# Kernel optimization log

Hardware: AMD Instinct MI355X
Metric: run time of the kernel (lower is better)

The kernel has to match this reference:

```python
import jax, jax.numpy as jnp
import numpy as np

N = 10000        # nodes
E = 160000       # graph edges (avg degree 16)
EI = 100000      # interaction edges
EP = 50000       # positive interaction edges
EA = 50000       # a2b edges
H, D = 4, 128    # GAT heads, per-head (and per-layer) dim
F_IN, F_EDGE = 39, 27   # 17+19+3 node feats, 27 edge feats
EMB = 256
FCN_IN = F_IN + 3 * D + D  # 551: x stacked with 3 GAT outputs + GCN output

PARAM_SHAPES = []
for l, fin in enumerate([F_IN, D, D]):
    PARAM_SHAPES += [(f"gat{l}_W", (fin, H * D)), (f"gat{l}_We", (F_EDGE, H * D)),
                     (f"gat{l}_asrc", (H, D)), (f"gat{l}_adst", (H, D)),
                     (f"gat{l}_aedge", (H, D)), (f"gat{l}_b", (D,))]
PARAM_SHAPES += [("gcn_W", (D, D)), ("gcn_b", (D,))]
for nm, fi, hh, fo in [("fcn", FCN_IN, 1024, EMB), ("link", 2 * EMB + 2, 1024, 1),
                       ("a2b", 2 * EMB, 1024, 6), ("node", EMB, 1024, 16),
                       ("int", 2 * EMB + 2, 1024, 3)]:
    PARAM_SHAPES += [(f"{nm}_W1", (fi, hh)), (f"{nm}_b1", (hh,)),
                     (f"{nm}_g", (hh,)), (f"{nm}_be", (hh,)),
                     (f"{nm}_W2", (hh, fo)), (f"{nm}_b2", (fo,))]
PARAM_NAMES = [n for n, _ in PARAM_SHAPES]


def setup_inputs():
    ks = jax.random.split(jax.random.key(0), len(PARAM_SHAPES) + 10)
    inp = {
        "x": jax.random.normal(ks[0], (N, F_IN), jnp.float32),
        "edge_index": jax.random.randint(ks[1], (2, E), 0, N),
        "edge_attr": jax.random.normal(ks[2], (E, F_EDGE), jnp.float32),
        "interaction_edge_index_pos": jax.random.randint(ks[3], (2, EP), 0, N),
        "interaction_edge_index": jax.random.randint(ks[4], (2, EI), 0, N),
        "xyz_data": jax.random.normal(ks[5], (N, 3), jnp.float32),
        "vector_data": jax.random.normal(ks[6], (N, 3), jnp.float32),
        "a2b_index": jax.random.randint(ks[7], (2, EA), 0, N),
        "mask": jnp.zeros((1,), jnp.float32),  # only used by the (disabled) evolver path
    }
    for i, (name, shp) in enumerate(PARAM_SHAPES):
        if name.endswith("_g"):
            inp[name] = jnp.ones(shp, jnp.float32)        # BatchNorm gamma
        elif name.endswith(("_be", "_b", "_b1", "_b2")):
            inp[name] = jnp.zeros(shp, jnp.float32)       # biases / BN beta
        else:
            inp[name] = jax.random.normal(ks[10 + i], shp, jnp.float32) * 0.05
    return inp


def _bn(h, g, b, eps=1e-5):
    # BatchNorm1d in training mode: biased batch statistics over axis 0
    m = h.mean(0)
    v = ((h - m) ** 2).mean(0)
    return (h - m) * jax.lax.rsqrt(v + eps) * g + b


def _seg_softmax(logits, seg, n):
    m = jax.ops.segment_max(logits, seg, num_segments=n)
    e = jnp.exp(logits - m[seg])
    s = jax.ops.segment_sum(e, seg, num_segments=n)
    return e / (s[seg] + 1e-16)


def _cos(a, b, eps=1e-8):
    na = jnp.maximum(jnp.sqrt((a * a).sum(1)), eps)
    nb = jnp.maximum(jnp.sqrt((b * b).sum(1)), eps)
    return (a * b).sum(1) / (na * nb)


def _forward(x, edge_attr, xyz_data, vector_data, edge_index, iep, iei, a2b_index, params):
    p = dict(zip(PARAM_NAMES, params))
    n = x.shape[0]
    src, dst = edge_index[0], edge_index[1]
    loops = jnp.arange(n)
    # GATConv add_self_loops with fill_value='mean': per-node mean of incoming edge_attr
    cnt = jax.ops.segment_sum(jnp.ones(src.shape[0], x.dtype), dst, num_segments=n)
    loop_attr = jax.ops.segment_sum(edge_attr, dst, num_segments=n) / jnp.maximum(cnt, 1.0)[:, None]
    src_a = jnp.concatenate([src, loops])
    dst_a = jnp.concatenate([dst, loops])
    ea_a = jnp.concatenate([edge_attr, loop_attr], 0)

    def gat(xx, W, We, asrc, adst, aedge, b):
        h = (xx @ W).reshape(n, H, D)
        a_s = (h * asrc).sum(-1)                               # [n,H]
        a_d = (h * adst).sum(-1)                               # [n,H]
        a_e = ((ea_a @ We).reshape(-1, H, D) * aedge).sum(-1)  # [E',H]
        alpha = jax.nn.leaky_relu(a_s[src_a] + a_d[dst_a] + a_e, 0.2)
        alpha = _seg_softmax(alpha, dst_a, n)                  # softmax over incoming edges
        out = jax.ops.segment_sum(h[src_a] * alpha[:, :, None], dst_a, num_segments=n)
        return out.mean(1) + b                                 # concat=False -> mean over heads

    out = x
    steps = [x]
    for l in range(3):
        out = jax.nn.relu(gat(out, p[f"gat{l}_W"], p[f"gat{l}_We"], p[f"gat{l}_asrc"],
                              p[f"gat{l}_adst"], p[f"gat{l}_aedge"], p[f"gat{l}_b"]))
        steps.append(out)
    # GCNConv: self loops (weight 1) + symmetric normalization
    deg = jax.ops.segment_sum(jnp.ones(dst_a.shape[0], x.dtype), dst_a, num_segments=n)
    dinv = jnp.where(deg > 0, deg ** -0.5, 0.0)
    norm = dinv[src_a] * dinv[dst_a]
    hg = out @ p["gcn_W"]
    out = jax.ops.segment_sum(hg[src_a] * norm[:, None], dst_a, num_segments=n) + p["gcn_b"]
    steps.append(out)

    feat = jnp.concatenate(steps, 1)                           # [n, 551]
    h = jax.nn.relu(feat @ p["fcn_W1"] + p["fcn_b1"])
    h = _bn(h, p["fcn_g"], p["fcn_be"])
    emb = jax.nn.relu(h @ p["fcn_W2"] + p["fcn_b2"])           # [n, 256]

    def head(z, nm):
        hh = jax.nn.relu(z @ p[f"{nm}_W1"] + p[f"{nm}_b1"])
        hh = _bn(hh, p[f"{nm}_g"], p[f"{nm}_be"])
        return hh @ p[f"{nm}_W2"] + p[f"{nm}_b2"]

    def pair_feat(idx):
        z = jnp.concatenate([emb[idx[0]], emb[idx[1]]], 1)
        d = ((xyz_data[idx[0]] - xyz_data[idx[1]]) ** 2).sum(1)  # squared distance (no sqrt)
        a = _cos(vector_data[idx[0]], vector_data[idx[1]])
        return jnp.concatenate([z, d[:, None], a[:, None]], 1)

    link_preds = head(pair_feat(iei), "link")
    a2b_preds = head(jnp.concatenate([emb[a2b_index[0]], emb[a2b_index[1]]], 1), "a2b")
    node_preds = head(emb, "node")
    int_preds = head(pair_feat(iep), "int")
    return (link_preds, a2b_preds, node_preds, int_preds)


def reference(x, edge_index, edge_attr, interaction_edge_index_pos, interaction_edge_index,
              xyz_data, vector_data, a2b_index, mask,
              gat0_W, gat0_We, gat0_asrc, gat0_adst, gat0_aedge, gat0_b,
              gat1_W, gat1_We, gat1_asrc, gat1_adst, gat1_aedge, gat1_b,
              gat2_W, gat2_We, gat2_asrc, gat2_adst, gat2_aedge, gat2_b,
              gcn_W, gcn_b,
              fcn_W1, fcn_b1, fcn_g, fcn_be, fcn_W2, fcn_b2,
              link_W1, link_b1, link_g, link_be, link_W2, link_b2,
              a2b_W1, a2b_b1, a2b_g, a2b_be, a2b_W2, a2b_b2,
              node_W1, node_b1, node_g, node_be, node_W2, node_b2,
              int_W1, int_b1, int_g, int_be, int_W2, int_b2):
    loc = locals()
    params = tuple(loc[nm] for nm in PARAM_NAMES)
    return _forward(x, edge_attr, xyz_data, vector_data, edge_index,
                    interaction_edge_index_pos, interaction_edge_index, a2b_index, params)
```

## Files before the change

kernel.cpp:

```cpp
#include <hip/hip_runtime.h>
#include <hip/hip_bf16.h>
#include <cstdint>
#include <cstddef>

typedef __attribute__((ext_vector_type(8))) short bf16x8;
typedef __attribute__((ext_vector_type(4))) float f32x4;

__device__ inline float bf2f(unsigned short u) {
    union { float f; unsigned int i; } c; c.i = ((unsigned int)u) << 16; return c.f;
}
__device__ inline unsigned short f2b(float v) {
    __hip_bfloat16 h = __float2bfloat16(v);
    union { __hip_bfloat16 b; unsigned short u; } c; c.b = h; return c.u;
}

__device__ inline float wmax64(float v) {
    #pragma unroll
    for (int o = 32; o; o >>= 1) v = fmaxf(v, __shfl_xor(v, o));
    return v;
}
__device__ inline float wsum64(float v) {
    #pragma unroll
    for (int o = 32; o; o >>= 1) v += __shfl_xor(v, o);
    return v;
// ... 33 lines not shown
            int idx = t * CH + j;
            if (idx < nn) coff[idx] = base + loc[j];
        }
    }
    if (t == 1023) coff[nn] = part[1023];
}

__global__ void k_fill(const int* __restrict__ dst, const int* __restrict__ coff,
                       int* __restrict__ fill, int* __restrict__ ceid, int E_) {
    int e = blockIdx.x * 256 + threadIdx.x;
    if (e < E_) {
        int d = dst[e];
        int p = atomicAdd(&fill[d], 1);
        ceid[coff[d] + p] = e;
    }
}

__global__ void k_copy_x(const float* __restrict__ x, float* __restrict__ feat, int nn) {
    int t = blockIdx.x * 256 + threadIdx.x;
    if (t < nn * 39) feat[(size_t)(t / 39) * 551 + (t % 39)] = x[t];
}

__global__ __launch_bounds__(128) void k_loopattr(const float* __restrict__ ea, const int* __restrict__ coff,
                                                  const int* __restrict__ ceid, float* __restrict__ la, int nn) {
    int g = blockIdx.x * 4 + (threadIdx.x >> 5);
    int lane = threadIdx.x & 31;
    if (g >= nn || lane >= 27) return;
    int beg = coff[g], cnt = coff[g + 1] - beg;
    float v = 0.f;
    for (int e = 0; e < cnt; ++e) v += ea[(size_t)ceid[beg + e] * 27 + lane];
// ... 15 lines not shown
    if (r >= E_ + nn) return;
    const float* src = (r < E_) ? (ea + (size_t)r * 27) : (la + (size_t)(r - E_) * 27);
    float o0 = 0, o1 = 0, o2 = 0, o3 = 0;
    #pragma unroll
    for (int f = 0; f < 27; ++f) {
        float xv = src[f];
        o0 += xv * Wea[f * 4 + 0];
        o1 += xv * Wea[f * 4 + 1];
        o2 += xv * Wea[f * 4 + 2];
        o3 += xv * Wea[f * 4 + 3];
    }
    a_e[(size_t)r * 4 + 0] = o0; a_e[(size_t)r * 4 + 1] = o1;
    a_e[(size_t)r * 4 + 2] = o2; a_e[(size_t)r * 4 + 3] = o3;
}

__global__ void k_asd(const float* __restrict__ h, const float* __restrict__ asrc,
                      const float* __restrict__ adst, float* __restrict__ a_s,
                      float* __restrict__ a_d, int nn) {
    int t = blockIdx.x * 256 + threadIdx.x;
    if (t >= nn * 4) return;
    int node = t >> 2, hh = t & 3;
    const float* hp = h + (size_t)node * 512 + hh * 128;
    float vs = 0.f, vd = 0.f;
    for (int d = 0; d < 128; ++d) {
        float xv = hp[d];
        vs += xv * asrc[hh * 128 + d];
        vd += xv * adst[hh * 128 + d];
    }
    a_s[t] = vs;
    a_d[t] = vd;
}

__global__ __launch_bounds__(64) void k_attn(
    const float* __restrict__ h, const float* __restrict__ a_s, const float* __restrict__ a_d,
    const float* __restrict__ a_e, const int* __restrict__ esrc,
    const int* __restrict__ coff, const int* __restrict__ ceid,
    const float* __restrict__ bvec, float* __restrict__ feat, int colofs, int E_) {
    const int i = blockIdx.x;
    const int lane = threadIdx.x;
    const int beg = coff[i];
    const int cnt = coff[i + 1] - beg;
    const int total = cnt + 1;
    const float d0 = a_d[i * 4 + 0], d1 = a_d[i * 4 + 1], d2 = a_d[i * 4 + 2], d3 = a_d[i * 4 + 3];
    float m0 = -1e30f, m1 = -1e30f, m2 = -1e30f, m3 = -1e30f;
    for (int e = lane; e < total; e += 64) {
        int eid, s;
        if (e < cnt) { eid = ceid[beg + e]; s = esrc[eid]; } else { eid = E_ + i; s = i; }
        float l0 = a_s[s * 4 + 0] + d0 + a_e[(size_t)eid * 4 + 0];
        float l1 = a_s[s * 4 + 1] + d1 + a_e[(size_t)eid * 4 + 1];
// ... 22 lines not shown
        s2 += __expf(l2 - m2); s3 += __expf(l3 - m3);
    }
    s0 = wsum64(s0); s1 = wsum64(s1); s2 = wsum64(s2); s3 = wsum64(s3);
    const int myh = lane >> 4;
    const float mm = myh == 0 ? m0 : myh == 1 ? m1 : myh == 2 ? m2 : m3;
    const float sv = myh == 0 ? s0 : myh == 1 ? s1 : myh == 2 ? s2 : s3;
    const float dd = myh == 0 ? d0 : myh == 1 ? d1 : myh == 2 ? d2 : d3;
    const float iv = 1.f / (sv + 1e-16f);
    float acc[8] = {0, 0, 0, 0, 0, 0, 0, 0};
    for (int e = 0; e < total; ++e) {
        int eid, s;
        if (e < cnt) { eid = ceid[beg + e]; s = esrc[eid]; } else { eid = E_ + i; s = i; }
        float l = a_s[s * 4 + myh] + dd + a_e[(size_t)eid * 4 + myh];
        l = l > 0.f ? l : 0.2f * l;
        const float wgt = __expf(l - mm) * iv;
        const float4* hp = (const float4*)(h + (size_t)s * 512 + lane * 8);
        float4 x0 = hp[0], x1 = hp[1];
        acc[0] += wgt * x0.x; acc[1] += wgt * x0.y; acc[2] += wgt * x0.z; acc[3] += wgt * x0.w;
        acc[4] += wgt * x1.x; acc[5] += wgt * x1.y; acc[6] += wgt * x1.z; acc[7] += wgt * x1.w;
    }
    __shared__ float sh[512];
    #pragma unroll
    for (int j = 0; j < 8; ++j) sh[lane * 8 + j] = acc[j];
    __syncthreads();
    #pragma unroll
    for (int r = 0; r < 2; ++r) {
        int d = lane * 2 + r;
        float v = 0.25f * (sh[d] + sh[128 + d] + sh[256 + d] + sh[384 + d]) + bvec[d];
        feat[(size_t)i * 551 + colofs + d] = fmaxf(v, 0.f);
    }
}

__global__ __launch_bounds__(64) void k_gcn(const float* __restrict__ hg, const int* __restrict__ esrc,
    const int* __restrict__ coff, const int* __restrict__ ceid, const int* __restrict__ indeg,
    const float* __restrict__ bvec, float* __restrict__ feat) {
    const int i = blockIdx.x;
    const int lane = threadIdx.x;
    const int beg = coff[i];
    const int cnt = coff[i + 1] - beg;
    const float di = rsqrtf((float)(indeg[i] + 1));
    const int d = lane * 2;
    float acc0 = hg[(size_t)i * 128 + d] * di;
    float acc1 = hg[(size_t)i * 128 + d + 1] * di;
    for (int e = 0; e < cnt; ++e) {
        int eid = ceid[beg + e];
        int s = esrc[eid];
        float ds = rsqrtf((float)(indeg[s] + 1));
        acc0 += hg[(size_t)s * 128 + d] * ds;
        acc1 += hg[(size_t)s * 128 + d + 1] * ds;
    }
    feat[(size_t)i * 551 + 423 + d] = acc0 * di + bvec[d];
    feat[(size_t)i * 551 + 423 + d + 1] = acc1 * di + bvec[d + 1];
}

__global__ void k_pack_ex(const int* __restrict__ idx, const float* __restrict__ xyz,
                          const float* __restrict__ vec, int4* __restrict__ pp, int P) {
    int p = blockIdx.x * 256 + threadIdx.x;
    if (p >= P) return;
    int i = idx[p], j = idx[P + p];
    float dx = xyz[i * 3] - xyz[j * 3];
    float dy = xyz[i * 3 + 1] - xyz[j * 3 + 1];
    float dz = xyz[i * 3 + 2] - xyz[j * 3 + 2];
    float d = dx * dx + dy * dy + dz * dz;
    float a0 = vec[i * 3], a1 = vec[i * 3 + 1], a2 = vec[i * 3 + 2];
    float b0 = vec[j * 3], b1 = vec[j * 3 + 1], b2 = vec[j * 3 + 2];
    float na = fmaxf(sqrtf(a0 * a0 + a1 * a1 + a2 * a2), 1e-8f);
    float nb = fmaxf(sqrtf(b0 * b0 + b1 * b1 + b2 * b2), 1e-8f);
    float a = (a0 * b0 + a1 * b1 + a2 * b2) / (na * nb);
    pp[p] = make_int4(i, j, __float_as_int(d), __float_as_int(a));
}

__global__ void k_pack2(const int* __restrict__ idx, int2* __restrict__ pp, int P) {
    int p = blockIdx.x * 256 + threadIdx.x;
    if (p >= P) return;
    pp[p] = make_int2(idx[p], idx[P + p]);
}

__global__ void k_stage_a(const float* __restrict__ src, int lds, int off,
                          unsigned short* __restrict__ dst, int ldd, int M, int K, int Mp) {
    int idx = blockIdx.x * 256 + threadIdx.x;
    if (idx >= Mp * ldd) return;
    int m = idx / ldd, k = idx - m * ldd;
    float v = (m < M && k < K) ? src[(size_t)m * lds + off + k] : 0.f;
    dst[idx] = f2b(v);
}

__global__ void k_conv_bt(const float* __restrict__ src, int ldn,
                          unsigned short* __restrict__ dst, int Kp, int K, int N, int Np) {
    int idx = blockIdx.x * 256 + threadIdx.x;
    if (idx >= Np * Kp) return;
    int nrow = idx / Kp, k = idx - nrow * Kp;
    float v = (nrow < N && k < K) ? src[(size_t)k * ldn + nrow] : 0.f;
    dst[idx] = f2b(v);
}

template<int OUT, bool RELU, bool BIAS>
__global__ __launch_bounds__(256) void gemm_mfma(
    const unsigned short* __restrict__ A, int lda,
    const unsigned short* __restrict__ Bt, int ldb,
    const float* __restrict__ bias,
    void* __restrict__ Cv, int ldc,
    int M, int N, int K) {
    const int t = threadIdx.x;
    const int lane = t & 63;
    const int wid = t >> 6;
    const int wm = wid >> 1, wn = wid & 1;
    const int bm0 = blockIdx.y * 128 + wm * 64;
// ... 93 lines not shown
        float wv = W2[(size_t)k * NO + c];
        W2f[(size_t)k * NO + c] = wv * s;
        accb += (be[k] - mv[k] * s) * wv;
    }
    red[t] = accb;
    __syncthreads();
    for (int o = 128; o; o >>= 1) {
        if (t < o) red[t] += red[t + o];
        __syncthreads();
    }
    if (t == 0) b2f[c] = b2[c] + red[0];
}

template<bool HASEX>
__global__ __launch_bounds__(256) void k_pairA(
    const unsigned short* __restrict__ u0, const unsigned short* __restrict__ u1,
    const float* __restrict__ b1, const float* __restrict__ W1ex,
    const int4* __restrict__ pp4, const int2* __restrict__ pp2,
    int P, float* __restrict__ part) {
    const int b = blockIdx.x, t = threadIdx.x;
    const int chunk = (P + 1023) / 1024;
    const int r0 = b * chunk;
    const int r1 = min(P, r0 + chunk);
    const float4 bb = *(const float4*)(b1 + t * 4);
    float4 wd = make_float4(0, 0, 0, 0), wa = make_float4(0, 0, 0, 0);
    if constexpr (HASEX) {
        wd = *(const float4*)(W1ex + t * 4);
        wa = *(const float4*)(W1ex + 1024 + t * 4);
    }
    float s[4] = {0, 0, 0, 0}, ss[4] = {0, 0, 0, 0};
    int r = r0;
    for (; r + 1 < r1; r += 2) {
        int i0A, i1A, i0B, i1B;
        float dA = 0, aA = 0, dB = 0, aB = 0;
        if constexpr (HASEX) {
            const int4 rA = pp4[r], rB = pp4[r + 1];
            i0A = rA.x; i1A = rA.y; dA = __int_as_float(rA.z); aA = __int_as_float(rA.w);
            i0B = rB.x; i1B = rB.y; dB = __int_as_float(rB.z); aB = __int_as_float(rB.w);
        } else {
            const int2 rA = pp2[r], rB = pp2[r + 1];
            i0A = rA.x; i1A = rA.y; i0B = rB.x; i1B = rB.y;
        }
        const ushort4 q0A = *(const ushort4*)(u0 + (size_t)i0A * 1024 + t * 4);
        const ushort4 q1A = *(const ushort4*)(u1 + (size_t)i1A * 1024 + t * 4);
        const ushort4 q0B = *(const ushort4*)(u0 + (size_t)i0B * 1024 + t * 4);
        const ushort4 q1B = *(const ushort4*)(u1 + (size_t)i1B * 1024 + t * 4);
        float hA[4], hB[4];
        hA[0] = bf2f(q0A.x) + bf2f(q1A.x) + bb.x;
        hA[1] = bf2f(q0A.y) + bf2f(q1A.y) + bb.y;
        hA[2] = bf2f(q0A.z) + bf2f(q1A.z) + bb.z;
        hA[3] = bf2f(q0A.w) + bf2f(q1A.w) + bb.w;
        hB[0] = bf2f(q0B.x) + bf2f(q1B.x) + bb.x;
        hB[1] = bf2f(q0B.y) + bf2f(q1B.y) + bb.y;
        hB[2] = bf2f(q0B.z) + bf2f(q1B.z) + bb.z;
        hB[3] = bf2f(q0B.w) + bf2f(q1B.w) + bb.w;
        if constexpr (HASEX) {
            hA[0] += dA * wd.x + aA * wa.x; hA[1] += dA * wd.y + aA * wa.y;
            hA[2] += dA * wd.z + aA * wa.z; hA[3] += dA * wd.w + aA * wa.w;
            hB[0] += dB * wd.x + aB * wa.x; hB[1] += dB * wd.y + aB * wa.y;
            hB[2] += dB * wd.z + aB * wa.z; hB[3] += dB * wd.w + aB * wa.w;
        }
        #pragma unroll
        for (int j = 0; j < 4; ++j) {
            float hvA = fmaxf(hA[j], 0.f);
            float hvB = fmaxf(hB[j], 0.f);
            s[j] += hvA + hvB; ss[j] += hvA * hvA + hvB * hvB;
        }
    }
    if (r < r1) {
        int i0, i1;
        float d = 0, a = 0;
        if constexpr (HASEX) {
            const int4 rA = pp4[r];
            i0 = rA.x; i1 = rA.y; d = __int_as_float(rA.z); a = __int_as_float(rA.w);
        } else {
            const int2 rA = pp2[r];
            i0 = rA.x; i1 = rA.y;
        }
        const ushort4 q0 = *(const ushort4*)(u0 + (size_t)i0 * 1024 + t * 4);
        const ushort4 q1 = *(const ushort4*)(u1 + (size_t)i1 * 1024 + t * 4);
        float h[4];
        h[0] = bf2f(q0.x) + bf2f(q1.x) + bb.x;
        h[1] = bf2f(q0.y) + bf2f(q1.y) + bb.y;
        h[2] = bf2f(q0.z) + bf2f(q1.z) + bb.z;
        h[3] = bf2f(q0.w) + bf2f(q1.w) + bb.w;
        if constexpr (HASEX) {
            h[0] += d * wd.x + a * wa.x; h[1] += d * wd.y + a * wa.y;
            h[2] += d * wd.z + a * wa.z; h[3] += d * wd.w + a * wa.w;
        }
        #pragma unroll
        for (int j = 0; j < 4; ++j) {
            float hv = fmaxf(h[j], 0.f);
            s[j] += hv; ss[j] += hv * hv;
        }
    }
    #pragma unroll
    for (int j = 0; j < 4; ++j) {
        part[(size_t)b * 2048 + t * 4 + j] = s[j];
        part[(size_t)b * 2048 + 1024 + t * 4 + j] = ss[j];
    }
}

template<int NO, bool HASEX>
__global__ __launch_bounds__(256) void k_pairB(
    const unsigned short* __restrict__ u0, const unsigned short* __restrict__ u1,
    const float* __restrict__ b1, const float* __restrict__ W1ex,
    const float* __restrict__ W2f, const float* __restrict__ b2f,
    const int4* __restrict__ pp4, const int2* __restrict__ pp2,
    float* __restrict__ out, int P) {
    const int t = threadIdx.x;
    const int wid = t >> 6, lane = t & 63;
    const int p0 = (blockIdx.x * 4 + wid) * 2;
    if (p0 >= P) return;
    const int p1 = p0 + 1;
    const bool has1 = p1 < P;
    int i0A, i1A, i0B, i1B;
    float dA = 0, aA = 0, dB = 0, aB = 0;
    if constexpr (HASEX) {
        const int4 rA = pp4[p0];
        const int4 rB = pp4[has1 ? p1 : p0];
        i0A = rA.x; i1A = rA.y; dA = __int_as_float(rA.z); aA = __int_as_float(rA.w);
        i0B = rB.x; i1B = rB.y; dB = __int_as_float(rB.z); aB = __int_as_float(rB.w);
    } else {
        const int2 rA = pp2[p0];
        const int2 rB = pp2[has1 ? p1 : p0];
        i0A = rA.x; i1A = rA.y; i0B = rB.x; i1B = rB.y;
    }
    const int k0 = lane * 16;
    union U { uint4 u; unsigned short us[8]; };
    U a0A, a1A, b0A, b1A_, a0B, a1B, b0B, b1B_;
    const unsigned short* pa = u0 + (size_t)i0A * 1024 + k0;
    const unsigned short* pb = u1 + (size_t)i1A * 1024 + k0;
    const unsigned short* pc = u0 + (size_t)i0B * 1024 + k0;
    const unsigned short* pd = u1 + (size_t)i1B * 1024 + k0;
    a0A.u = *(const uint4*)(pa);     a1A.u = *(const uint4*)(pa + 8);
    b0A.u = *(const uint4*)(pb);     b1A_.u = *(const uint4*)(pb + 8);
    a0B.u = *(const uint4*)(pc);     a1B.u = *(const uint4*)(pc + 8);
    b0B.u = *(const uint4*)(pd);     b1B_.u = *(const uint4*)(pd + 8);
    float4 bbv[4];
    #pragma unroll
    for (int q = 0; q < 4; ++q) bbv[q] = *(const float4*)(b1 + k0 + q * 4);
    float4 wdv[4], wav[4];
    if constexpr (HASEX) {
        #pragma unroll
        for (int q = 0; q < 4; ++q) {
            wdv[q] = *(const float4*)(W1ex + k0 + q * 4);
            wav[q] = *(const float4*)(W1ex + 1024 + k0 + q * 4);
        }
    }
// ... 2 lines not shown
    for (int no = 0; no < NO; ++no) { accA[no] = 0.f; accB[no] = 0.f; }
    #pragma unroll
    for (int j = 0; j < 16; ++j) {
        const int q = j >> 2, c = j & 3;
        const float bbj = (&bbv[q].x)[c];
        float exA = 0.f, exB = 0.f;
        if constexpr (HASEX) {
            const float wdj = (&wdv[q].x)[c], waj = (&wav[q].x)[c];
            exA = dA * wdj + aA * waj;
            exB = dB * wdj + aB * waj;
        }
        const float hAv = (j < 8 ? bf2f(a0A.us[j]) : bf2f(a1A.us[j - 8]))
                        + (j < 8 ? bf2f(b0A.us[j]) : bf2f(b1A_.us[j - 8])) + bbj + exA;
        const float hBv = (j < 8 ? bf2f(a0B.us[j]) : bf2f(a1B.us[j - 8]))
                        + (j < 8 ? bf2f(b0B.us[j]) : bf2f(b1B_.us[j - 8])) + bbj + exB;
        const float rA = fmaxf(hAv, 0.f);
        const float rB = fmaxf(hBv, 0.f);
        const int kk = k0 + j;
        #pragma unroll
        for (int no = 0; no < NO; ++no) {
            const float wv = W2f[(size_t)kk * NO + no];
            accA[no] += rA * wv;
            accB[no] += rB * wv;
        }
    }
    #pragma unroll
    for (int no = 0; no < NO; ++no) {
        float vA = accA[no], vB = accB[no];
        #pragma unroll
        for (int o = 32; o; o >>= 1) { vA += __shfl_down(vA, o); vB += __shfl_down(vB, o); }
        if (lane == 0) {
            out[(size_t)p0 * NO + no] = vA + b2f[no];
            if (has1) out[(size_t)p1 * NO + no] = vB + b2f[no];
        }
    }
}

extern "C" void kernel_launch(void* const* d_in, const int* in_sizes, int n_in,
                              void* d_out, int out_size, void* d_ws, size_t ws_size,
                              hipStream_t stream) {
    (void)n_in; (void)out_size; (void)ws_size;
    const float* x     = (const float*)d_in[0];
    const int*   eidx  = (const int*)d_in[1];
    const float* eattr = (const float*)d_in[2];
    const int*   iep   = (const int*)d_in[3];
    const int*   iei   = (const int*)d_in[4];
    const float* xyz   = (const float*)d_in[5];
    const float* vecd  = (const float*)d_in[6];
// ... 29 lines not shown
        hp[hh] = {(const float*)d_in[base], (const float*)d_in[base + 1], (const float*)d_in[base + 2],
                  (const float*)d_in[base + 3], (const float*)d_in[base + 4], (const float*)d_in[base + 5]};
    }

    char* w = (char*)d_ws;
    size_t off = 0;
    auto alloc = [&](size_t bytes) -> void* {
        void* p = w + off;
        off = (off + bytes + 255) & ~(size_t)255;
        return p;
    };
    int* indeg   = (int*)alloc((size_t)n * 4);
    int* fill    = (int*)alloc((size_t)n * 4);
    int* coff    = (int*)alloc((size_t)(n + 1) * 4);
    int* ceid    = (int*)alloc((size_t)E_ * 4);
    int4* ppL    = (int4*)alloc((size_t)EIn * 16);
    int2* ppA    = (int2*)alloc((size_t)EAn * 8);
    int4* ppI    = (int4*)alloc((size_t)EPn * 16);
    float* lattr = (float*)alloc((size_t)n * 27 * 4);
    float* Wea   = (float*)alloc(27 * 4 * 4);
    float* a_e   = (float*)alloc((size_t)(E_ + n) * 4 * 4);
    float* a_s   = (float*)alloc((size_t)n * 4 * 4);
    float* a_d   = (float*)alloc((size_t)n * 4 * 4);
    float* part  = (float*)alloc((size_t)1024 * 2048 * 4);
    float* tmp   = (float*)alloc((size_t)32 * 2048 * 4);
    float* mv    = (float*)alloc(2048 * 4);
    float* W2f   = (float*)alloc((size_t)1024 * 256 * 4);
    float* b2f   = (float*)alloc(256 * 4);
    float* feat  = (float*)alloc((size_t)n * 551 * 4);
    float* hbuf  = (float*)alloc((size_t)n * 512 * 4);
    unsigned short* Ab   = (unsigned short*)alloc((size_t)Mp * 576 * 2);
    unsigned short* hidb = (unsigned short*)alloc((size_t)Mp * 1024 * 2);
    unsigned short* embb = (unsigned short*)alloc((size_t)Mp * 256 * 2);
    unsigned short* u0b  = (unsigned short*)alloc((size_t)n * 1024 * 2);
    unsigned short* u1b  = (unsigned short*)alloc((size_t)n * 1024 * 2);
    unsigned short* btB  = (unsigned short*)alloc((size_t)1024 * 1024 * 2);

    hipMemsetAsync(indeg, 0, (size_t)n * 4, stream);
    hipMemsetAsync(fill, 0, (size_t)n * 4, stream);
    hipMemsetAsync(hidb + (size_t)n * 1024, 0, (size_t)(Mp - n) * 1024 * 2, stream);
    hipMemsetAsync(embb + (size_t)n * 256, 0, (size_t)(Mp - n) * 256 * 2, stream);

    const int NCH = 32;
    auto stats_finish = [&](int M, int NB) {
        dim3 g1(8, NCH);
        k_red1<<<g1, 256, 0, stream>>>(part, tmp, NB, NCH);
        k_red2<<<4, 256, 0, stream>>>(tmp, mv, M, NCH);
    };
    auto stageA = [&](const float* src, int lds, int colofs, int K, int Kp) {
        int tot = Mp * Kp;
        k_stage_a<<<(tot + 255) / 256, 256, 0, stream>>>(src, lds, colofs, Ab, Kp, n, K, Mp);
    };
    auto convBt = [&](const float* src, int ldn, int K, int Kp, int N, int Np) {
        int tot = Np * Kp;
        k_conv_bt<<<(tot + 255) / 256, 256, 0, stream>>>(src, ldn, btB, Kp, K, N, Np);
    };

    const int* dsta = eidx + E_;
    k_count<<<(E_ + 255) / 256, 256, 0, stream>>>(dsta, indeg, E_);
    k_scan<<<1, 1024, 0, stream>>>(indeg, coff, n);
    k_fill<<<(E_ + 255) / 256, 256, 0, stream>>>(dsta, coff, fill, ceid, E_);
    k_copy_x<<<((n * 39) + 255) / 256, 256, 0, stream>>>(x, feat, n);
    k_loopattr<<<(n + 3) / 4, 128, 0, stream>>>(eattr, coff, ceid, lattr, n);
    k_pack_ex<<<(EIn + 255) / 256, 256, 0, stream>>>(iei, xyz, vecd, ppL, EIn);
    k_pack2<<<(EAn + 255) / 256, 256, 0, stream>>>(a2bi, ppA, EAn);
    k_pack_ex<<<(EPn + 255) / 256, 256, 0, stream>>>(iep, xyz, vecd, ppI, EPn);

    const int colofs_in[3] = {0, 39, 167};
    const int fin[3] = {39, 128, 128};
    const int finp[3] = {64, 128, 128};
    for (int l = 0; l < 3; ++l) {
        k_wea<<<1, 128, 0, stream>>>(gatWe[l], gatAe[l], Wea);
        stageA(feat, 551, colofs_in[l], fin[l], finp[l]);
        convBt(gatW[l], 512, fin[l], finp[l], 512, 512);
        dim3 g(4, MB);
        gemm_mfma<0, false, false><<<g, 256, 0, stream>>>(Ab, finp[l], btB, finp[l], nullptr, hbuf, 512, n, 512, finp[l]);
        k_ae<<<(E_ + n + 255) / 256, 256, 0, stream>>>(eattr, lattr, Wea, a_e, E_, n);
        k_asd<<<(n * 4 + 255) / 256, 256, 0, stream>>>(hbuf, gatAs[l], gatAd[l], a_s, a_d, n);
        k_attn<<<n, 64, 0, stream>>>(hbuf, a_s, a_d, a_e, eidx, coff, ceid, gatB[l], feat, 39 + 128 * l, E_);
    }
    {
        stageA(feat, 551, 295, 128, 128);
        convBt(gcnW, 128, 128, 128, 128, 128);
        dim3 g(1, MB);
        gemm_mfma<0, false, false><<<g, 256, 0, stream>>>(Ab, 128, btB, 128, nullptr, hbuf, 128, n, 128, 128);
        k_gcn<<<n, 64, 0, stream>>>(hbuf, eidx, coff, ceid, indeg, gcnB, feat);
    }
    {
        stageA(feat, 551, 0, 551, 576);
        convBt(fcnW1, 1024, 551, 576, 1024, 1024);
        dim3 g(8, MB);
        gemm_mfma<1, true, true><<<g, 256, 0, stream>>>(Ab, 576, btB, 576, fcnB1, hidb, 1024, n, 1024, 576);
        k_stats1b<<<256, 256, 0, stream>>>(hidb, n, part);
        stats_finish(n, 256);
        k_fold<<<256, 256, 0, stream>>>(fcnW2, fcnG, fcnBe, fcnB2, mv, W2f, b2f, 256);
        convBt(W2f, 256, 1024, 1024, 256, 256);
        dim3 g2(2, MB);
        gemm_mfma<1, true, true><<<g2, 256, 0, stream>>>(hidb, 1024, btB, 1024, b2f, embb, 256, n, 256, 1024);
    }

    float* out = (float*)d_out;
    float* out_link = out;
    float* out_a2b  = out + (size_t)EIn;
    float* out_node = out_a2b + (size_t)EAn * 6;
    float* out_int  = out_node + (size_t)n * 16;

    const dim3 gu(8, MB);

    {
        convBt(hp[0].W1, 1024, 256, 256, 1024, 1024);
        gemm_mfma<1, false, false><<<gu, 256, 0, stream>>>(embb, 256, btB, 256, nullptr, u0b, 1024, n, 1024, 256);
        convBt(hp[0].W1 + (size_t)256 * 1024, 1024, 256, 256, 1024, 1024);
        gemm_mfma<1, false, false><<<gu, 256, 0, stream>>>(embb, 256, btB, 256, nullptr, u1b, 1024, n, 1024, 256);
        const float* W1ex = hp[0].W1 + (size_t)512 * 1024;
        k_pairA<true><<<1024, 256, 0, stream>>>(u0b, u1b, hp[0].b1, W1ex, ppL, nullptr, EIn, part);
        stats_finish(EIn, 1024);
        k_fold<<<1, 256, 0, stream>>>(hp[0].W2, hp[0].g, hp[0].be, hp[0].b2, mv, W2f, b2f, 1);
        k_pairB<1, true><<<(EIn + 7) / 8, 256, 0, stream>>>(u0b, u1b, hp[0].b1, W1ex, W2f, b2f, ppL, nullptr, out_link, EIn);
    }
    {
        convBt(hp[1].W1, 1024, 256, 256, 1024, 1024);
        gemm_mfma<1, false, false><<<gu, 256, 0, stream>>>(embb, 256, btB, 256, nullptr, u0b, 1024, n, 1024, 256);
        convBt(hp[1].W1 + (size_t)256 * 1024, 1024, 256, 256, 1024, 1024);
        gemm_mfma<1, false, false><<<gu, 256, 0, stream>>>(embb, 256, btB, 256, nullptr, u1b, 1024, n, 1024, 256);
        k_pairA<false><<<1024, 256, 0, stream>>>(u0b, u1b, hp[1].b1, nullptr, nullptr, ppA, EAn, part);
        stats_finish(EAn, 1024);
        k_fold<<<6, 256, 0, stream>>>(hp[1].W2, hp[1].g, hp[1].be, hp[1].b2, mv, W2f, b2f, 6);
        k_pairB<6, false><<<(EAn + 7) / 8, 256, 0, stream>>>(u0b, u1b, hp[1].b1, nullptr, W2f, b2f, nullptr, ppA, out_a2b, EAn);
    }
    {
        convBt(hp[2].W1, 1024, 256, 256, 1024, 1024);
        gemm_mfma<1, true, true><<<gu, 256, 0, stream>>>(embb, 256, btB, 256, hp[2].b1, hidb, 1024, n, 1024, 256);
        k_stats1b<<<256, 256, 0, stream>>>(hidb, n, part);
        stats_finish(n, 256);
        k_fold<<<16, 256, 0, stream>>>(hp[2].W2, hp[2].g, hp[2].be, hp[2].b2, mv, W2f, b2f, 16);
        convBt(W2f, 16, 1024, 1024, 16, 128);
        dim3 g2(1, MB);
        gemm_mfma<0, false, true><<<g2, 256, 0, stream>>>(hidb, 1024, btB, 1024, b2f, out_node, 16, n, 16, 1024);
    }
    {
        convBt(hp[3].W1, 1024, 256, 256, 1024, 1024);
        gemm_mfma<1, false, false><<<gu, 256, 0, stream>>>(embb, 256, btB, 256, nullptr, u0b, 1024, n, 1024, 256);
        convBt(hp[3].W1 + (size_t)256 * 1024, 1024, 256, 256, 1024, 1024);
        gemm_mfma<1, false, false><<<gu, 256, 0, stream>>>(embb, 256, btB, 256, nullptr, u1b, 1024, n, 1024, 256);
        const float* W1ex = hp[3].W1 + (size_t)512 * 1024;
        k_pairA<true><<<1024, 256, 0, stream>>>(u0b, u1b, hp[3].b1, W1ex, ppI, nullptr, EPn, part);
        stats_finish(EPn, 1024);
        k_fold<<<3, 256, 0, stream>>>(hp[3].W2, hp[3].g, hp[3].be, hp[3].b2, mv, W2f, b2f, 3);
        k_pairB<3, true><<<(EPn + 7) / 8, 256, 0, stream>>>(u0b, u1b, hp[3].b1, W1ex, W2f, b2f, ppI, nullptr, out_int, EPn);
    }
}
```

Before: 1.279 ms.

## Store GAT/GCN features in bf16, fuse pair GEMMs, bucket pairs by source node

GAT and GCN projection outputs are now written as bf16 and read as bf16 in the attention, score and aggregation kernels, halving gather bandwidth. The two per-head first-layer GEMMs (u0, u1) are merged into one 2048-wide GEMM with interleaved output, so only one weight conversion and one launch are needed. Pair lists are counting-sorted by first node and results are scattered back through a permutation, which improves cache locality of the u0 row gathers. The cost is extra count, scan and pack launches per head, atomics-driven nondeterministic ordering within buckets (which can change reduction order in the stats), and reduced precision of the intermediate features.

```diff
diff --git a/kernel.cpp b/kernel.cpp
--- a/kernel.cpp
+++ b/kernel.cpp
@@ -71,6 +71,31 @@
         int p = atomicAdd(&fill[d], 1);
         ceid[coff[d] + p] = e;
     }
+}
+
+template<bool HASEX>
+__global__ void k_pack_sorted(const int* __restrict__ idx, const float* __restrict__ xyz,
+                              const float* __restrict__ vec, const int* __restrict__ poff,
+                              int* __restrict__ pfill, int4* __restrict__ spp,
+                              int* __restrict__ sord, int P) {
+    int p = blockIdx.x * 256 + threadIdx.x;
+    if (p >= P) return;
+    int i = idx[p], j = idx[P + p];
+    float d = 0.f, a = 0.f;
+    if constexpr (HASEX) {
+        float dx = xyz[i * 3] - xyz[j * 3];
+        float dy = xyz[i * 3 + 1] - xyz[j * 3 + 1];
+        float dz = xyz[i * 3 + 2] - xyz[j * 3 + 2];
+        d = dx * dx + dy * dy + dz * dz;
+        float a0 = vec[i * 3], a1 = vec[i * 3 + 1], a2 = vec[i * 3 + 2];
+        float b0 = vec[j * 3], b1 = vec[j * 3 + 1], b2 = vec[j * 3 + 2];
+        float na = fmaxf(sqrtf(a0 * a0 + a1 * a1 + a2 * a2), 1e-8f);
+        float nb = fmaxf(sqrtf(b0 * b0 + b1 * b1 + b2 * b2), 1e-8f);
+        a = (a0 * b0 + a1 * b1 + a2 * b2) / (na * nb);
+    }
+    int pos = poff[i] + atomicAdd(&pfill[i], 1);
+    spp[pos] = make_int4(i, j, __float_as_int(d), __float_as_int(a));
+    sord[pos] = p;
 }
 
 __global__ void k_copy_x(const float* __restrict__ x, float* __restrict__ feat, int nn) {
@@ -116,25 +141,31 @@
     a_e[(size_t)r * 4 + 2] = o2; a_e[(size_t)r * 4 + 3] = o3;
 }
 
-__global__ void k_asd(const float* __restrict__ h, const float* __restrict__ asrc,
+__global__ void k_asd(const unsigned short* __restrict__ hb, const float* __restrict__ asrc,
                       const float* __restrict__ adst, float* __restrict__ a_s,
                       float* __restrict__ a_d, int nn) {
     int t = blockIdx.x * 256 + threadIdx.x;
     if (t >= nn * 4) return;
     int node = t >> 2, hh = t & 3;
-    const float* hp = h + (size_t)node * 512 + hh * 128;
+    const unsigned short* hp = hb + (size_t)node * 512 + hh * 128;
     float vs = 0.f, vd = 0.f;
-    for (int d = 0; d < 128; ++d) {
-        float xv = hp[d];
-        vs += xv * asrc[hh * 128 + d];
-        vd += xv * adst[hh * 128 + d];
+    #pragma unroll
+    for (int q = 0; q < 16; ++q) {
+        union { uint4 u; unsigned short us[8]; } c;
+        c.u = *(const uint4*)(hp + q * 8);
+        #pragma unroll
+        for (int j = 0; j < 8; ++j) {
+            float xv = bf2f(c.us[j]);
+            vs += xv * asrc[hh * 128 + q * 8 + j];
+            vd += xv * adst[hh * 128 + q * 8 + j];
+        }
     }
     a_s[t] = vs;
     a_d[t] = vd;
 }
 
 __global__ __launch_bounds__(64) void k_attn(
-    const float* __restrict__ h, const float* __restrict__ a_s, const float* __restrict__ a_d,
+    const unsigned short* __restrict__ hb, const float* __restrict__ a_s, const float* __restrict__ a_d,
     const float* __restrict__ a_e, const int* __restrict__ esrc,
     const int* __restrict__ coff, const int* __restrict__ ceid,
     const float* __restrict__ bvec, float* __restrict__ feat, int colofs, int E_) {
@@ -187,10 +218,10 @@
         float l = a_s[s * 4 + myh] + dd + a_e[(size_t)eid * 4 + myh];
         l = l > 0.f ? l : 0.2f * l;
         const float wgt = __expf(l - mm) * iv;
-        const float4* hp = (const float4*)(h + (size_t)s * 512 + lane * 8);
-        float4 x0 = hp[0], x1 = hp[1];
-        acc[0] += wgt * x0.x; acc[1] += wgt * x0.y; acc[2] += wgt * x0.z; acc[3] += wgt * x0.w;
-        acc[4] += wgt * x1.x; acc[5] += wgt * x1.y; acc[6] += wgt * x1.z; acc[7] += wgt * x1.w;
+        union { uint4 u; unsigned short us[8]; } c;
+        c.u = *(const uint4*)(hb + (size_t)s * 512 + lane * 8);
+        #pragma unroll
+        for (int j = 0; j < 8; ++j) acc[j] += wgt * bf2f(c.us[j]);
     }
     __shared__ float sh[512];
     #pragma unroll
@@ -204,7 +235,7 @@
     }
 }
 
-__global__ __launch_bounds__(64) void k_gcn(const float* __restrict__ hg, const int* __restrict__ esrc,
+__global__ __launch_bounds__(64) void k_gcn(const unsigned short* __restrict__ hg, const int* __restrict__ esrc,
     const int* __restrict__ coff, const int* __restrict__ ceid, const int* __restrict__ indeg,
     const float* __restrict__ bvec, float* __restrict__ feat) {
     const int i = blockIdx.x;
@@ -213,40 +244,19 @@
     const int cnt = coff[i + 1] - beg;
     const float di = rsqrtf((float)(indeg[i] + 1));
     const int d = lane * 2;
-    float acc0 = hg[(size_t)i * 128 + d] * di;
-    float acc1 = hg[(size_t)i * 128 + d + 1] * di;
+    unsigned int u0 = *(const unsigned int*)(hg + (size_t)i * 128 + d);
+    float acc0 = bf2f((unsigned short)(u0 & 0xffff)) * di;
+    float acc1 = bf2f((unsigned short)(u0 >> 16)) * di;
     for (int e = 0; e < cnt; ++e) {
         int eid = ceid[beg + e];
         int s = esrc[eid];
         float ds = rsqrtf((float)(indeg[s] + 1));
-        acc0 += hg[(size_t)s * 128 + d] * ds;
-        acc1 += hg[(size_t)s * 128 + d + 1] * ds;
+        unsigned int u = *(const unsigned int*)(hg + (size_t)s * 128 + d);
+        acc0 += bf2f((unsigned short)(u & 0xffff)) * ds;
+        acc1 += bf2f((unsigned short)(u >> 16)) * ds;
     }
     feat[(size_t)i * 551 + 423 + d] = acc0 * di + bvec[d];
     feat[(size_t)i * 551 + 423 + d + 1] = acc1 * di + bvec[d + 1];
-}
-
-__global__ void k_pack_ex(const int* __restrict__ idx, const float* __restrict__ xyz,
-                          const float* __restrict__ vec, int4* __restrict__ pp, int P) {
-    int p = blockIdx.x * 256 + threadIdx.x;
-    if (p >= P) return;
-    int i = idx[p], j = idx[P + p];
-    float dx = xyz[i * 3] - xyz[j * 3];
-    float dy = xyz[i * 3 + 1] - xyz[j * 3 + 1];
-    float dz = xyz[i * 3 + 2] - xyz[j * 3 + 2];
-    float d = dx * dx + dy * dy + dz * dz;
-    float a0 = vec[i * 3], a1 = vec[i * 3 + 1], a2 = vec[i * 3 + 2];
-    float b0 = vec[j * 3], b1 = vec[j * 3 + 1], b2 = vec[j * 3 + 2];
-    float na = fmaxf(sqrtf(a0 * a0 + a1 * a1 + a2 * a2), 1e-8f);
-    float nb = fmaxf(sqrtf(b0 * b0 + b1 * b1 + b2 * b2), 1e-8f);
-    float a = (a0 * b0 + a1 * b1 + a2 * b2) / (na * nb);
-    pp[p] = make_int4(i, j, __float_as_int(d), __float_as_int(a));
-}
-
-__global__ void k_pack2(const int* __restrict__ idx, int2* __restrict__ pp, int P) {
-    int p = blockIdx.x * 256 + threadIdx.x;
-    if (p >= P) return;
-    pp[p] = make_int2(idx[p], idx[P + p]);
 }
 
 __global__ void k_stage_a(const float* __restrict__ src, int lds, int off,
@@ -264,6 +274,15 @@
     if (idx >= Np * Kp) return;
     int nrow = idx / Kp, k = idx - nrow * Kp;
     float v = (nrow < N && k < K) ? src[(size_t)k * ldn + nrow] : 0.f;
+    dst[idx] = f2b(v);
+}
+
+__global__ void k_conv_bt2(const float* __restrict__ W1, unsigned short* __restrict__ dst) {
+    int idx = blockIdx.x * 256 + threadIdx.x;
+    if (idx >= 2048 * 256) return;
+    int nrow = idx >> 8, k = idx & 255;
+    float v = (nrow < 1024) ? W1[(size_t)k * 1024 + nrow]
+                            : W1[(size_t)(256 + k) * 1024 + (nrow - 1024)];
     dst[idx] = f2b(v);
 }
 
@@ -387,9 +406,9 @@
 
 template<bool HASEX>
 __global__ __launch_bounds__(256) void k_pairA(
-    const unsigned short* __restrict__ u0, const unsigned short* __restrict__ u1,
+    const unsigned short* __restrict__ u0, const unsigned short* __restrict__ u1, int ldu,
     const float* __restrict__ b1, const float* __restrict__ W1ex,
-    const int4* __restrict__ pp4, const int2* __restrict__ pp2,
+    const int4* __restrict__ spp,
     int P, float* __restrict__ part) {
     const int b = blockIdx.x, t = threadIdx.x;
     const int chunk = (P + 1023) / 1024;
@@ -404,20 +423,17 @@
     float s[4] = {0, 0, 0, 0}, ss[4] = {0, 0, 0, 0};
     int r = r0;
     for (; r + 1 < r1; r += 2) {
-        int i0A, i1A, i0B, i1B;
+        const int4 rA = spp[r], rB = spp[r + 1];
+        const int i0A = rA.x, i1A = rA.y, i0B = rB.x, i1B = rB.y;
         float dA = 0, aA = 0, dB = 0, aB = 0;
         if constexpr (HASEX) {
-            const int4 rA = pp4[r], rB = pp4[r + 1];
-            i0A = rA.x; i1A = rA.y; dA = __int_as_float(rA.z); aA = __int_as_float(rA.w);
-            i0B = rB.x; i1B = rB.y; dB = __int_as_float(rB.z); aB = __int_as_float(rB.w);
-        } else {
-            const int2 rA = pp2[r], rB = pp2[r + 1];
-            i0A = rA.x; i1A = rA.y; i0B = rB.x; i1B = rB.y;
-        }
-        const ushort4 q0A = *(const ushort4*)(u0 + (size_t)i0A * 1024 + t * 4);
-        const ushort4 q1A = *(const ushort4*)(u1 + (size_t)i1A * 1024 + t * 4);
-        const ushort4 q0B = *(const ushort4*)(u0 + (size_t)i0B * 1024 + t * 4);
-        const ushort4 q1B = *(const ushort4*)(u1 + (size_t)i1B * 1024 + t * 4);
+            dA = __int_as_float(rA.z); aA = __int_as_float(rA.w);
+            dB = __int_as_float(rB.z); aB = __int_as_float(rB.w);
+        }
+        const ushort4 q0A = *(const ushort4*)(u0 + (size_t)i0A * ldu + t * 4);
+        const ushort4 q1A = *(const ushort4*)(u1 + (size_t)i1A * ldu + t * 4);
+        const ushort4 q0B = *(const ushort4*)(u0 + (size_t)i0B * ldu + t * 4);
+        const ushort4 q1B = *(const ushort4*)(u1 + (size_t)i1B * ldu + t * 4);
         float hA[4], hB[4];
         hA[0] = bf2f(q0A.x) + bf2f(q1A.x) + bb.x;
         hA[1] = bf2f(q0A.y) + bf2f(q1A.y) + bb.y;
@@ -441,17 +457,12 @@
         }
     }
     if (r < r1) {
-        int i0, i1;
+        const int4 rA = spp[r];
+        const int i0 = rA.x, i1 = rA.y;
         float d = 0, a = 0;
-        if constexpr (HASEX) {
-            const int4 rA = pp4[r];
-            i0 = rA.x; i1 = rA.y; d = __int_as_float(rA.z); a = __int_as_float(rA.w);
-        } else {
-            const int2 rA = pp2[r];
-            i0 = rA.x; i1 = rA.y;
-        }
-        const ushort4 q0 = *(const ushort4*)(u0 + (size_t)i0 * 1024 + t * 4);
-        const ushort4 q1 = *(const ushort4*)(u1 + (size_t)i1 * 1024 + t * 4);
+        if constexpr (HASEX) { d = __int_as_float(rA.z); a = __int_as_float(rA.w); }
+        const ushort4 q0 = *(const ushort4*)(u0 + (size_t)i0 * ldu + t * 4);
+        const ushort4 q1 = *(const ushort4*)(u1 + (size_t)i1 * ldu + t * 4);
         float h[4];
         h[0] = bf2f(q0.x) + bf2f(q1.x) + bb.x;
         h[1] = bf2f(q0.y) + bf2f(q1.y) + bb.y;
@@ -476,10 +487,10 @@
 
 template<int NO, bool HASEX>
 __global__ __launch_bounds__(256) void k_pairB(
-    const unsigned short* __restrict__ u0, const unsigned short* __restrict__ u1,
+    const unsigned short* __restrict__ u0, const unsigned short* __restrict__ u1, int ldu,
     const float* __restrict__ b1, const float* __restrict__ W1ex,
     const float* __restrict__ W2f, const float* __restrict__ b2f,
-    const int4* __restrict__ pp4, const int2* __restrict__ pp2,
+    const int4* __restrict__ spp, const int* __restrict__ sord,
     float* __restrict__ out, int P) {
     const int t = threadIdx.x;
     const int wid = t >> 6, lane = t & 63;
@@ -487,25 +498,21 @@
     if (p0 >= P) return;
     const int p1 = p0 + 1;
     const bool has1 = p1 < P;
-    int i0A, i1A, i0B, i1B;
+    const int4 rA = spp[p0];
+    const int4 rB = spp[has1 ? p1 : p0];
+    const int i0A = rA.x, i1A = rA.y, i0B = rB.x, i1B = rB.y;
     float dA = 0, aA = 0, dB = 0, aB = 0;
     if constexpr (HASEX) {
-        const int4 rA = pp4[p0];
-        const int4 rB = pp4[has1 ? p1 : p0];
-        i0A = rA.x; i1A = rA.y; dA = __int_as_float(rA.z); aA = __int_as_float(rA.w);
-        i0B = rB.x; i1B = rB.y; dB = __int_as_float(rB.z); aB = __int_as_float(rB.w);
-    } else {
-        const int2 rA = pp2[p0];
-        const int2 rB = pp2[has1 ? p1 : p0];
-        i0A = rA.x; i1A = rA.y; i0B = rB.x; i1B = rB.y;
+        dA = __int_as_float(rA.z); aA = __int_as_float(rA.w);
+        dB = __int_as_float(rB.z); aB = __int_as_float(rB.w);
     }
     const int k0 = lane * 16;
     union U { uint4 u; unsigned short us[8]; };
     U a0A, a1A, b0A, b1A_, a0B, a1B, b0B, b1B_;
-    const unsigned short* pa = u0 + (size_t)i0A * 1024 + k0;
-    const unsigned short* pb = u1 + (size_t)i1A * 1024 + k0;
-    const unsigned short* pc = u0 + (size_t)i0B * 1024 + k0;
-    const unsigned short* pd = u1 + (size_t)i1B * 1024 + k0;
+    const unsigned short* pa = u0 + (size_t)i0A * ldu + k0;
+    const unsigned short* pb = u1 + (size_t)i1A * ldu + k0;
+    const unsigned short* pc = u0 + (size_t)i0B * ldu + k0;
+    const unsigned short* pd = u1 + (size_t)i1B * ldu + k0;
     a0A.u = *(const uint4*)(pa);     a1A.u = *(const uint4*)(pa + 8);
     b0A.u = *(const uint4*)(pb);     b1A_.u = *(const uint4*)(pb + 8);
     a0B.u = *(const uint4*)(pc);     a1B.u = *(const uint4*)(pc + 8);
@@ -538,24 +545,26 @@
                         + (j < 8 ? bf2f(b0A.us[j]) : bf2f(b1A_.us[j - 8])) + bbj + exA;
         const float hBv = (j < 8 ? bf2f(a0B.us[j]) : bf2f(a1B.us[j - 8]))
                         + (j < 8 ? bf2f(b0B.us[j]) : bf2f(b1B_.us[j - 8])) + bbj + exB;
-        const float rA = fmaxf(hAv, 0.f);
-        const float rB = fmaxf(hBv, 0.f);
+        const float rAv = fmaxf(hAv, 0.f);
+        const float rBv = fmaxf(hBv, 0.f);
         const int kk = k0 + j;
         #pragma unroll
         for (int no = 0; no < NO; ++no) {
             const float wv = W2f[(size_t)kk * NO + no];
-            accA[no] += rA * wv;
-            accB[no] += rB * wv;
-        }
-    }
+            accA[no] += rAv * wv;
+            accB[no] += rBv * wv;
+        }
+    }
+    const int oA = sord[p0];
+    const int oB = has1 ? sord[p1] : 0;
     #pragma unroll
     for (int no = 0; no < NO; ++no) {
         float vA = accA[no], vB = accB[no];
         #pragma unroll
         for (int o = 32; o; o >>= 1) { vA += __shfl_down(vA, o); vB += __shfl_down(vB, o); }
         if (lane == 0) {
-            out[(size_t)p0 * NO + no] = vA + b2f[no];
-            if (has1) out[(size_t)p1 * NO + no] = vB + b2f[no];
+            out[(size_t)oA * NO + no] = vA + b2f[no];
+            if (has1) out[(size_t)oB * NO + no] = vB + b2f[no];
         }
     }
 }
@@ -615,9 +624,11 @@
     int* fill    = (int*)alloc((size_t)n * 4);
     int* coff    = (int*)alloc((size_t)(n + 1) * 4);
     int* ceid    = (int*)alloc((size_t)E_ * 4);
-    int4* ppL    = (int4*)alloc((size_t)EIn * 16);
-    int2* ppA    = (int2*)alloc((size_t)EAn * 8);
-    int4* ppI    = (int4*)alloc((size_t)EPn * 16);
+    int* pcnt    = (int*)alloc((size_t)n * 4);
+    int* pfill   = (int*)alloc((size_t)n * 4);
+    int* poff    = (int*)alloc((size_t)(n + 1) * 4);
+    int4* spp    = (int4*)alloc((size_t)EIn * 16);
+    int* sord    = (int*)alloc((size_t)EIn * 4);
     float* lattr = (float*)alloc((size_t)n * 27 * 4);
     float* Wea   = (float*)alloc(27 * 4 * 4);
     float* a_e   = (float*)alloc((size_t)(E_ + n) * 4 * 4);
@@ -629,13 +640,12 @@
     float* W2f   = (float*)alloc((size_t)1024 * 256 * 4);
     float* b2f   = (float*)alloc(256 * 4);
     float* feat  = (float*)alloc((size_t)n * 551 * 4);
-    float* hbuf  = (float*)alloc((size_t)n * 512 * 4);
+    unsigned short* hb   = (unsigned short*)alloc((size_t)n * 512 * 2);
     unsigned short* Ab   = (unsigned short*)alloc((size_t)Mp * 576 * 2);
     unsigned short* hidb = (unsigned short*)alloc((size_t)Mp * 1024 * 2);
     unsigned short* embb = (unsigned short*)alloc((size_t)Mp * 256 * 2);
-    unsigned short* u0b  = (unsigned short*)alloc((size_t)n * 1024 * 2);
-    unsigned short* u1b  = (unsigned short*)alloc((size_t)n * 1024 * 2);
-    unsigned short* btB  = (unsigned short*)alloc((size_t)1024 * 1024 * 2);
+    unsigned short* u01b = (unsigned short*)alloc((size_t)n * 2048 * 2);
+    unsigned short* btB  = (unsigned short*)alloc((size_t)2048 * 256 * 2 > (size_t)1024 * 1024 * 2 ? (size_t)2048 * 1024 * 2 : (size_t)2048 * 1024 * 2);
 
     hipMemsetAsync(indeg, 0, (size_t)n * 4, stream);
     hipMemsetAsync(fill, 0, (size_t)n * 4, stream);
@@ -656,6 +666,16 @@
         int tot = Np * Kp;
         k_conv_bt<<<(tot + 255) / 256, 256, 0, stream>>>(src, ldn, btB, Kp, K, N, Np);
     };
+    auto bucket_pairs = [&](const int* pidx, int P, bool hasex) {
+        hipMemsetAsync(pcnt, 0, (size_t)n * 4, stream);
+        hipMemsetAsync(pfill, 0, (size_t)n * 4, stream);
+        k_count<<<(P + 255) / 256, 256, 0, stream>>>(pidx, pcnt, P);
+        k_scan<<<1, 1024, 0, stream>>>(pcnt, poff, n);
+        if (hasex)
+            k_pack_sorted<true><<<(P + 255) / 256, 256, 0, stream>>>(pidx, xyz, vecd, poff, pfill, spp, sord, P);
+        else
+            k_pack_sorted<false><<<(P + 255) / 256, 256, 0, stream>>>(pidx, xyz, vecd, poff, pfill, spp, sord, P);
+    };
 
     const int* dsta = eidx + E_;
     k_count<<<(E_ + 255) / 256, 256, 0, stream>>>(dsta, indeg, E_);
@@ -663,9 +683,6 @@
     k_fill<<<(E_ + 255) / 256, 256, 0, stream>>>(dsta, coff, fill, ceid, E_);
     k_copy_x<<<((n * 39) + 255) / 256, 256, 0, stream>>>(x, feat, n);
     k_loopattr<<<(n + 3) / 4, 128, 0, stream>>>(eattr, coff, ceid, lattr, n);
-    k_pack_ex<<<(EIn + 255) / 256, 256, 0, stream>>>(iei, xyz, vecd, ppL, EIn);
-    k_pack2<<<(EAn + 255) / 256, 256, 0, stream>>>(a2bi, ppA, EAn);
-    k_pack_ex<<<(EPn + 255) / 256, 256, 0, stream>>>(iep, xyz, vecd, ppI, EPn);
 
     const int colofs_in[3] = {0, 39, 167};
     const int fin[3] = {39, 128, 128};
@@ -675,17 +692,17 @@
         stageA(feat, 551, colofs_in[l], fin[l], finp[l]);
         convBt(gatW[l], 512, fin[l], finp[l], 512, 512);
         dim3 g(4, MB);
-        gemm_mfma<0, false, false><<<g, 256, 0, stream>>>(Ab, finp[l], btB, finp[l], nullptr, hbuf, 512, n, 512, finp[l]);
+        gemm_mfma<1, false, false><<<g, 256, 0, stream>>>(Ab, finp[l], btB, finp[l], nullptr, hb, 512, n, 512, finp[l]);
         k_ae<<<(E_ + n + 255) / 256, 256, 0, stream>>>(eattr, lattr, Wea, a_e, E_, n);
-        k_asd<<<(n * 4 + 255) / 256, 256, 0, stream>>>(hbuf, gatAs[l], gatAd[l], a_s, a_d, n);
-        k_attn<<<n, 64, 0, stream>>>(hbuf, a_s, a_d, a_e, eidx, coff, ceid, gatB[l], feat, 39 + 128 * l, E_);
+        k_asd<<<(n * 4 + 255) / 256, 256, 0, stream>>>(hb, gatAs[l], gatAd[l], a_s, a_d, n);
+        k_attn<<<n, 64, 0, stream>>>(hb, a_s, a_d, a_e, eidx, coff, ceid, gatB[l], feat, 39 + 128 * l, E_);
     }
     {
         stageA(feat, 551, 295, 128, 128);
         convBt(gcnW, 128, 128, 128, 128, 128);
         dim3 g(1, MB);
-        gemm_mfma<0, false, false><<<g, 256, 0, stream>>>(Ab, 128, btB, 128, nullptr, hbuf, 128, n, 128, 128);
-        k_gcn<<<n, 64, 0, stream>>>(hbuf, eidx, coff, ceid, indeg, gcnB, feat);
+        gemm_mfma<1, false, false><<<g, 256, 0, stream>>>(Ab, 128, btB, 128, nullptr, hb, 128, n, 128, 128);
+        k_gcn<<<n, 64, 0, stream>>>(hb, eidx, coff, ceid, indeg, gcnB, feat);
     }
     {
         stageA(feat, 551, 0, 551, 576);
@@ -706,31 +723,30 @@
     float* out_node = out_a2b + (size_t)EAn * 6;
     float* out_int  = out_node + (size_t)n * 16;
 
-    const dim3 gu(8, MB);
+    const dim3 gu2(16, MB);
 
     {
-        convBt(hp[0].W1, 1024, 256, 256, 1024, 1024);
-        gemm_mfma<1, false, false><<<gu, 256, 0, stream>>>(embb, 256, btB, 256, nullptr, u0b, 1024, n, 1024, 256);
-        convBt(hp[0].W1 + (size_t)256 * 1024, 1024, 256, 256, 1024, 1024);
-        gemm_mfma<1, false, false><<<gu, 256, 0, stream>>>(embb, 256, btB, 256, nullptr, u1b, 1024, n, 1024, 256);
+        k_conv_bt2<<<(2048 * 256 + 255) / 256, 256, 0, stream>>>(hp[0].W1, btB);
+        gemm_mfma<1, false, false><<<gu2, 256, 0, stream>>>(embb, 256, btB, 256, nullptr, u01b, 2048, n, 2048, 256);
         const float* W1ex = hp[0].W1 + (size_t)512 * 1024;
-        k_pairA<true><<<1024, 256, 0, stream>>>(u0b, u1b, hp[0].b1, W1ex, ppL, nullptr, EIn, part);
+        bucket_pairs(iei, EIn, true);
+        k_pairA<true><<<1024, 256, 0, stream>>>(u01b, u01b + 1024, 2048, hp[0].b1, W1ex, spp, EIn, part);
         stats_finish(EIn, 1024);
         k_fold<<<1, 256, 0, stream>>>(hp[0].W2, hp[0].g, hp[0].be, hp[0].b2, mv, W2f, b2f, 1);
-        k_pairB<1, true><<<(EIn + 7) / 8, 256, 0, stream>>>(u0b, u1b, hp[0].b1, W1ex, W2f, b2f, ppL, nullptr, out_link, EIn);
+        k_pairB<1, true><<<(EIn + 7) / 8, 256, 0, stream>>>(u01b, u01b + 1024, 2048, hp[0].b1, W1ex, W2f, b2f, spp, sord, out_link, EIn);
     }
     {
-        convBt(hp[1].W1, 1024, 256, 256, 1024, 1024);
-        gemm_mfma<1, false, false><<<gu, 256, 0, stream>>>(embb, 256, btB, 256, nullptr, u0b, 1024, n, 1024, 256);
-        convBt(hp[1].W1 + (size_t)256 * 1024, 1024, 256, 256, 1024, 1024);
-        gemm_mfma<1, false, false><<<gu, 256, 0, stream>>>(embb, 256, btB, 256, nullptr, u1b, 1024, n, 1024, 256);
-        k_pairA<false><<<1024, 256, 0, stream>>>(u0b, u1b, hp[1].b1, nullptr, nullptr, ppA, EAn, part);
+        k_conv_bt2<<<(2048 * 256 + 255) / 256, 256, 0, stream>>>(hp[1].W1, btB);
+        gemm_mfma<1, false, false><<<gu2, 256, 0, stream>>>(embb, 256, btB, 256, nullptr, u01b, 2048, n, 2048, 256);
+        bucket_pairs(a2bi, EAn, false);
+        k_pairA<false><<<1024, 256, 0, stream>>>(u01b, u01b + 1024, 2048, hp[1].b1, nullptr, spp, EAn, part);
         stats_finish(EAn, 1024);
         k_fold<<<6, 256, 0, stream>>>(hp[1].W2, hp[1].g, hp[1].be, hp[1].b2, mv, W2f, b2f, 6);
-        k_pairB<6, false><<<(EAn + 7) / 8, 256, 0, stream>>>(u0b, u1b, hp[1].b1, nullptr, W2f, b2f, nullptr, ppA, out_a2b, EAn);
+        k_pairB<6, false><<<(EAn + 7) / 8, 256, 0, stream>>>(u01b, u01b + 1024, 2048, hp[1].b1, nullptr, W2f, b2f, spp, sord, out_a2b, EAn);
     }
     {
         convBt(hp[2].W1, 1024, 256, 256, 1024, 1024);
+        dim3 gu(8, MB);
         gemm_mfma<1, true, true><<<gu, 256, 0, stream>>>(embb, 256, btB, 256, hp[2].b1, hidb, 1024, n, 1024, 256);
         k_stats1b<<<256, 256, 0, stream>>>(hidb, n, part);
         stats_finish(n, 256);
@@ -740,14 +756,13 @@
         gemm_mfma<0, false, true><<<g2, 256, 0, stream>>>(hidb, 1024, btB, 1024, b2f, out_node, 16, n, 16, 1024);
     }
     {
-        convBt(hp[3].W1, 1024, 256, 256, 1024, 1024);
-        gemm_mfma<1, false, false><<<gu, 256, 0, stream>>>(embb, 256, btB, 256, nullptr, u0b, 1024, n, 1024, 256);
-        convBt(hp[3].W1 + (size_t)256 * 1024, 1024, 256, 256, 1024, 1024);
-        gemm_mfma<1, false, false><<<gu, 256, 0, stream>>>(embb, 256, btB, 256, nullptr, u1b, 1024, n, 1024, 256);
+        k_conv_bt2<<<(2048 * 256 + 255) / 256, 256, 0, stream>>>(hp[3].W1, btB);
+        gemm_mfma<1, false, false><<<gu2, 256, 0, stream>>>(embb, 256, btB, 256, nullptr, u01b, 2048, n, 2048, 256);
         const float* W1ex = hp[3].W1 + (size_t)512 * 1024;
-        k_pairA<true><<<1024, 256, 0, stream>>>(u0b, u1b, hp[3].b1, W1ex, ppI, nullptr, EPn, part);
+        bucket_pairs(iep, EPn, true);
+        k_pairA<true><<<1024, 256, 0, stream>>>(u01b, u01b + 1024, 2048, hp[3].b1, W1ex, spp, EPn, part);
         stats_finish(EPn, 1024);
         k_fold<<<3, 256, 0, stream>>>(hp[3].W2, hp[3].g, hp[3].be, hp[3].b2, mv, W2f, b2f, 3);
-        k_pairB<3, true><<<(EPn + 7) / 8, 256, 0, stream>>>(u0b, u1b, hp[3].b1, W1ex, W2f, b2f, ppI, nullptr, out_int, EPn);
-    }
-}
+        k_pairB<3, true><<<(EPn + 7) / 8, 256, 0, stream>>>(u01b, u01b + 1024, 2048, hp[3].b1, W1ex, W2f, b2f, spp, sord, out_int, EPn);
+    }
+}
```

Result: faster. 1.180 ms (-7.8%).
